# Kernel tuning notes

Measured on AMD Instinct MI355X. Metric: run time of the kernel, lower is better.

Reference implementation:

```python
import jax, jax.numpy as jnp
import numpy as np

EPS = 1e-6
ENERGY_THRESHOLD = 0.95
LS_INIT = 1e-5


def setup_inputs() -> dict:
    key = jax.random.key(0)
    k_x, k_u, k_s, k_v = jax.random.split(key, 4)
    dim, max_rank = 4096, 16
    x = jax.random.normal(k_x, (4, 2048, dim), dtype=jnp.float32)
    U = jax.random.normal(k_u, (dim, max_rank), dtype=jnp.float32) * 0.02
    S = jax.random.uniform(k_s, (max_rank,), dtype=jnp.float32)
    V = jax.random.normal(k_v, (max_rank, dim), dtype=jnp.float32) * 0.02
    norm_weight = jnp.ones((dim,), dtype=jnp.float32)
    gamma = jnp.full((dim,), LS_INIT, dtype=jnp.float32)
    return {"x": x, "U": U, "S": S, "V": V,
            "norm_weight": norm_weight, "gamma": gamma}


def _rank_mask(S):
    # Effective rank from singular-value energy (non-differentiable decision,
    # matching torch's .item() host sync which detaches it from autograd).
    s_abs = jnp.abs(S)
    cum = jnp.cumsum(s_abs) / jnp.maximum(s_abs.sum(), 1e-8)
    hit = cum >= ENERGY_THRESHOLD
    r = jnp.where(hit.any(), jnp.argmax(hit) + 1, S.shape[0])
    keep = (jnp.arange(S.shape[0]) < r).astype(S.dtype)
    return jax.lax.stop_gradient(keep)


def reference(x, U, S, V, norm_weight, gamma):
    # RMSNorm (computed in fp32, matching x.float() in torch)
    xf = x.astype(jnp.float32)
    x_norm = (xf * jax.lax.rsqrt(jnp.mean(xf * xf, axis=-1, keepdims=True) + EPS)).astype(x.dtype)
    x_norm = x_norm * norm_weight
    # Adaptive-rank low-rank projection: masking columns >= r equals slicing [:r]
    keep = _rank_mask(S)
    h = jnp.einsum('bsd,dr->bsr', x_norm, U)        # [B,S,max_rank]
    h = h * (S * keep)                               # zero out ranks >= r
    h = jnp.einsum('bsr,rd->bsd', h, V)             # [B,S,dim]
    # LayerScale + residual
    return x + h * gamma
```

## Files before the change

kernel.cpp:

```cpp
#include <hip/hip_runtime.h>

#define DIM   4096
#define RANK  16
#define ROWS  4
#define NT    512
#define NWAVE 8

typedef __fp16 f16;
typedef __fp16 f16x2 __attribute__((ext_vector_type(2)));
typedef __fp16 f16x4 __attribute__((ext_vector_type(4)));
typedef __fp16 f16x8 __attribute__((ext_vector_type(8)));
typedef int    int2v  __attribute__((ext_vector_type(2)));
typedef float  f32x4v __attribute__((ext_vector_type(4)));

__device__ __forceinline__ float fdot2f(f16x2 a, f16x2 b, float c) {
    return __builtin_amdgcn_fdot2(a, b, c, false);
}

__device__ __forceinline__ f16x2 h2get(const int4& v, int i) {
    int w;
    switch (i) { case 0: w = v.x; break; case 1: w = v.y; break;
                 case 2: w = v.z; break; default: w = v.w; }
    return __builtin_bit_cast(f16x2, w);
}

__global__ __launch_bounds__(256) void prep_weights(const float* __restrict__ U,
                                                    const float* __restrict__ nw,
                                                    const float* __restrict__ V,
                                                    f16* __restrict__ Ut,
                                                    f16* __restrict__ Vp) {
    const int d = blockIdx.x * 256 + threadIdx.x;
    const float wv = nw[d];
    const float4* U4 = (const float4*)U;
    const float4 u0 = U4[(size_t)d * 4 + 0];
    const float4 u1 = U4[(size_t)d * 4 + 1];
    const float4 u2 = U4[(size_t)d * 4 + 2];
    const float4 u3 = U4[(size_t)d * 4 + 3];
    Ut[ 0*DIM + d] = (f16)(u0.x*wv); Ut[ 1*DIM + d] = (f16)(u0.y*wv);
    Ut[ 2*DIM + d] = (f16)(u0.z*wv); Ut[ 3*DIM + d] = (f16)(u0.w*wv);
    Ut[ 4*DIM + d] = (f16)(u1.x*wv); Ut[ 5*DIM + d] = (f16)(u1.y*wv);
    Ut[ 6*DIM + d] = (f16)(u1.z*wv); Ut[ 7*DIM + d] = (f16)(u1.w*wv);
    Ut[ 8*DIM + d] = (f16)(u2.x*wv); Ut[ 9*DIM + d] = (f16)(u2.y*wv);
    Ut[10*DIM + d] = (f16)(u2.z*wv); Ut[11*DIM + d] = (f16)(u2.w*wv);
    Ut[12*DIM + d] = (f16)(u3.x*wv); Ut[13*DIM + d] = (f16)(u3.y*wv);
    Ut[14*DIM + d] = (f16)(u3.z*wv); Ut[15*DIM + d] = (f16)(u3.w*wv);
    f16 vq[16];
    #pragma unroll
    for (int q = 0; q < 16; ++q) vq[q] = (f16)V[(size_t)q * DIM + d];
    f16x8 lo = { vq[0], vq[1], vq[2], vq[3], vq[4], vq[5], vq[6], vq[7] };
    f16x8 hi = { vq[8], vq[9], vq[10], vq[11], vq[12], vq[13], vq[14], vq[15] };
    f16x8* Vp8 = (f16x8*)Vp;
    Vp8[(size_t)d * 2 + 0] = lo;
    Vp8[(size_t)d * 2 + 1] = hi;
}

__global__ __launch_bounds__(NT, 6) void arl_fused(
    const float* __restrict__ x,  const f16* __restrict__ Ut,
    const float* __restrict__ S,  const f16* __restrict__ Vp,
    const float* __restrict__ gamma, float* __restrict__ out)
{
    const int t    = threadIdx.x;
    const int w    = t >> 6;
    const int lane = t & 63;
    const int rg   = w & 3;
    const int dh   = w >> 2;
    const size_t row0 = (size_t)blockIdx.x * ROWS;

    const float4* x4   = (const float4*)(x + row0 * DIM);
    float4*       out4 = (float4*)(out + row0 * DIM);
    const int4*   Ut16 = (const int4*)Ut;
    const int4*   Vp16 = (const int4*)Vp;
    const float4* g4   = (const float4*)gamma;

    __shared__ __align__(16) f16 xh[ROWS * DIM];
    __shared__ float s_ssq[NWAVE][ROWS];
    __shared__ float s_hraw[NWAVE][16];
    __shared__ __align__(16) f16 s_hh[ROWS * RANK];

    float ssqp[ROWS] = {0.f, 0.f, 0.f, 0.f};
    #pragma unroll
    for (int i = 0; i < 8; ++i) {
        const int idx = i * NT + t;
        const int r   = i >> 1;
        const float4 val = x4[idx];
        ssqp[r] = fmaf(val.x, val.x, ssqp[r]);
        ssqp[r] = fmaf(val.y, val.y, ssqp[r]);
        ssqp[r] = fmaf(val.z, val.z, ssqp[r]);
        ssqp[r] = fmaf(val.w, val.w, ssqp[r]);
        f16x4 pk;
        pk.x = (f16)val.x; pk.y = (f16)val.y; pk.z = (f16)val.z; pk.w = (f16)val.w;
        ((f16x4*)xh)[idx] = pk;
    }
    __syncthreads();

    #pragma unroll
    for (int r = 0; r < ROWS; ++r) {
        float s = ssqp[r];
        #pragma unroll
        for (int off = 32; off >= 1; off >>= 1) s += __shfl_xor(s, off, 64);
        if (lane == 0) s_ssq[w][r] = s;
    }

    float v[16];
    #pragma unroll
    for (int i = 0; i < 16; ++i) v[i] = 0.f;

    #pragma unroll 1
    for (int k = 0; k < 4; ++k) {
        const int p = dh * 256 + k * 64 + lane;
        int4 u[4];
        #pragma unroll
        for (int ql = 0; ql < 4; ++ql)
            u[ql] = Ut16[(size_t)(rg * 4 + ql) * 512 + p];
        int4 xr[ROWS];
        #pragma unroll
        for (int r = 0; r < ROWS; ++r) xr[r] = ((const int4*)xh)[r * 512 + p];
        #pragma unroll
        for (int i = 0; i < 4; ++i) {
            f16x2 xp[ROWS];
            #pragma unroll
            for (int r = 0; r < ROWS; ++r) xp[r] = h2get(xr[r], i);
            #pragma unroll
            for (int ql = 0; ql < 4; ++ql) {
                const f16x2 up = h2get(u[ql], i);
                #pragma unroll
                for (int r = 0; r < ROWS; ++r)
                    v[r*4+ql] = fdot2f(xp[r], up, v[r*4+ql]);
            }
        }
    }

    #pragma unroll
    for (int i = 0; i < 8; ++i) {
        int a = __float_as_int(v[2*i]);
        int b = __float_as_int(v[2*i+1]);
        int2v pr = __builtin_amdgcn_permlane32_swap(a, b, false, false);
        v[i] = __int_as_float(pr.x) + __int_as_float(pr.y);
    }
    #pragma unroll
    for (int s = 1; s <= 3; ++s) {
        const int off = 32 >> s;
        const int n   = 8 >> s;
        const bool hi = (lane >> (5 - s)) & 1;
        #pragma unroll
        for (int i = 0; i < n; ++i) {
            float lo = v[2*i], hg = v[2*i+1];
            float slo = __shfl_xor(lo, off, 64);
            float shg = __shfl_xor(hg, off, 64);
            v[i] = hi ? (hg + shg) : (lo + slo);
        }
    }
    v[0] += __shfl_xor(v[0], 2, 64);
    v[0] += __shfl_xor(v[0], 1, 64);
    {
        const int idx = ((lane >> 5) & 1) | (((lane >> 4) & 1) << 1)
                      | (((lane >> 3) & 1) << 2) | (((lane >> 2) & 1) << 3);
        if ((lane & 3) == 0) s_hraw[w][idx] = v[0];
    }
    __syncthreads();

    if (t < 64) {
        const int r = t >> 4, q = t & 15;
        const int qg = q >> 2, ql = q & 3;
        const float hs = s_hraw[qg][r * 4 + ql] + s_hraw[qg + 4][r * 4 + ql];
        float tot_ssq = 0.f;
        #pragma unroll
        for (int ww = 0; ww < NWAVE; ++ww) tot_ssq += s_ssq[ww][r];
        const float rstd = rsqrtf(tot_ssq * (1.0f / DIM) + 1e-6f);
        float tot = 0.f;
        #pragma unroll
        for (int i = 0; i < RANK; ++i) tot += fabsf(S[i]);
        const float denom = fmaxf(tot, 1e-8f);
        float cum = 0.f, se = 0.f;
        #pragma unroll
        for (int i = 0; i < RANK; ++i) {
            if (i == q) se = ((cum / denom) < 0.95f) ? S[i] : 0.f;
            cum += fabsf(S[i]);
        }
        s_hh[t] = (f16)(hs * se * rstd);
    }
    __syncthreads();

    f16x2 hp[ROWS][8];
    {
        const int4* hh16 = (const int4*)s_hh;
        #pragma unroll
        for (int r = 0; r < ROWS; ++r) {
            const int4 a = hh16[r*2 + 0];
            const int4 b = hh16[r*2 + 1];
            #pragma unroll
            for (int i = 0; i < 4; ++i) {
                hp[r][i]     = h2get(a, i);
                hp[r][4 + i] = h2get(b, i);
            }
        }
    }
    #pragma unroll 1
    for (int k = 0; k < 2; ++k) {
        const int c = k * NT + t;
        float4 xr[ROWS];
        #pragma unroll
        for (int r = 0; r < ROWS; ++r) xr[r] = x4[(size_t)r * (DIM/4) + c];
        const float4 g = g4[c];
        float acc[ROWS][4];
        #pragma unroll
        for (int r = 0; r < ROWS; ++r)
            #pragma unroll
            for (int j = 0; j < 4; ++j) acc[r][j] = 0.f;
        #pragma unroll
        for (int j = 0; j < 4; ++j) {
            const int dd = c * 4 + j;
            const int4 v0 = Vp16[(size_t)dd * 2 + 0];
            const int4 v1 = Vp16[(size_t)dd * 2 + 1];
            #pragma unroll
            for (int r = 0; r < ROWS; ++r) {
                float a = acc[r][j];
                #pragma unroll
                for (int i = 0; i < 4; ++i)
                    a = fdot2f(hp[r][i], h2get(v0, i), a);
                #pragma unroll
                for (int i = 0; i < 4; ++i)
                    a = fdot2f(hp[r][4+i], h2get(v1, i), a);
                acc[r][j] = a;
            }
        }
        #pragma unroll
        for (int r = 0; r < ROWS; ++r) {
            float4 o;
            o.x = fmaf(g.x, acc[r][0], xr[r].x);
            o.y = fmaf(g.y, acc[r][1], xr[r].y);
            o.z = fmaf(g.z, acc[r][2], xr[r].z);
            o.w = fmaf(g.w, acc[r][3], xr[r].w);
            __builtin_nontemporal_store(*(const f32x4v*)&o,
                                        (f32x4v*)(out4 + (size_t)r * (DIM/4) + c));
        }
    }
}

extern "C" void kernel_launch(void* const* d_in, const int* in_sizes, int n_in,
                              void* d_out, int out_size, void* d_ws, size_t ws_size,
                              hipStream_t stream) {
    (void)in_sizes; (void)n_in; (void)ws_size;
    const float* x  = (const float*)d_in[0];
    const float* U  = (const float*)d_in[1];
    const float* S  = (const float*)d_in[2];
    const float* V  = (const float*)d_in[3];
    const float* nw = (const float*)d_in[4];
    const float* g  = (const float*)d_in[5];
    float* out = (float*)d_out;
    f16* Ut = (f16*)d_ws;
    f16* Vp = (f16*)((char*)d_ws + 16 * DIM * sizeof(f16));

    hipLaunchKernelGGL(prep_weights, dim3(DIM / 256), dim3(256), 0, stream,
                       U, nw, V, Ut, Vp);

    const int rows = out_size / DIM;
    const int grid = rows / ROWS;
    hipLaunchKernelGGL(arl_fused, dim3(grid), dim3(NT), 0, stream,
                       x, Ut, S, Vp, g, out);
}
```

Before: 85.33 us.

## Split fused kernel into projection and apply kernels, prefetch U tiles

Splits the single fused kernel in two. The first computes the normalized rank-16 projection h per row and writes it to a workspace. The second, with 256 threads per block, re-reads x and applies V, gamma and the residual. It also software-prefetches the next U tile inside the projection loop. The split is meant to free LDS and registers so more blocks fit per CU, at the cost of reading x from global memory a second time and adding a kernel launch.

New measurement: 87.41 us. 1.02x slower.

```diff
diff --git a/kernel.cpp b/kernel.cpp
--- a/kernel.cpp
+++ b/kernel.cpp
@@ -4,6 +4,7 @@
 #define RANK  16
 #define ROWS  4
 #define NT    512
+#define NTB   256
 #define NWAVE 8
 
 typedef __fp16 f16;
@@ -54,10 +55,9 @@
     Vp8[(size_t)d * 2 + 1] = hi;
 }
 
-__global__ __launch_bounds__(NT, 6) void arl_fused(
+__global__ __launch_bounds__(NT, 6) void arl_h(
     const float* __restrict__ x,  const f16* __restrict__ Ut,
-    const float* __restrict__ S,  const f16* __restrict__ Vp,
-    const float* __restrict__ gamma, float* __restrict__ out)
+    const float* __restrict__ S,  f16* __restrict__ hWS)
 {
     const int t    = threadIdx.x;
     const int w    = t >> 6;
@@ -67,15 +67,19 @@
     const size_t row0 = (size_t)blockIdx.x * ROWS;
 
     const float4* x4   = (const float4*)(x + row0 * DIM);
-    float4*       out4 = (float4*)(out + row0 * DIM);
     const int4*   Ut16 = (const int4*)Ut;
-    const int4*   Vp16 = (const int4*)Vp;
-    const float4* g4   = (const float4*)gamma;
 
     __shared__ __align__(16) f16 xh[ROWS * DIM];
     __shared__ float s_ssq[NWAVE][ROWS];
     __shared__ float s_hraw[NWAVE][16];
-    __shared__ __align__(16) f16 s_hh[ROWS * RANK];
+
+    int4 u[4];
+    {
+        const int p0 = dh * 256 + lane;
+        #pragma unroll
+        for (int ql = 0; ql < 4; ++ql)
+            u[ql] = Ut16[(size_t)(rg * 4 + ql) * 512 + p0];
+    }
 
     float ssqp[ROWS] = {0.f, 0.f, 0.f, 0.f};
     #pragma unroll
@@ -107,11 +111,12 @@
 
     #pragma unroll 1
     for (int k = 0; k < 4; ++k) {
+        const int pn = dh * 256 + ((k + 1) & 3) * 64 + lane;
+        int4 un[4];
+        #pragma unroll
+        for (int ql = 0; ql < 4; ++ql)
+            un[ql] = Ut16[(size_t)(rg * 4 + ql) * 512 + pn];
         const int p = dh * 256 + k * 64 + lane;
-        int4 u[4];
-        #pragma unroll
-        for (int ql = 0; ql < 4; ++ql)
-            u[ql] = Ut16[(size_t)(rg * 4 + ql) * 512 + p];
         int4 xr[ROWS];
         #pragma unroll
         for (int r = 0; r < ROWS; ++r) xr[r] = ((const int4*)xh)[r * 512 + p];
@@ -128,6 +133,8 @@
                     v[r*4+ql] = fdot2f(xp[r], up, v[r*4+ql]);
             }
         }
+        #pragma unroll
+        for (int ql = 0; ql < 4; ++ql) u[ql] = un[ql];
     }
 
     #pragma unroll
@@ -177,27 +184,39 @@
             if (i == q) se = ((cum / denom) < 0.95f) ? S[i] : 0.f;
             cum += fabsf(S[i]);
         }
-        s_hh[t] = (f16)(hs * se * rstd);
-    }
-    __syncthreads();
+        hWS[(row0 + r) * RANK + q] = (f16)(hs * se * rstd);
+    }
+}
+
+__global__ __launch_bounds__(NTB, 6) void arl_apply(
+    const float* __restrict__ x,  const f16* __restrict__ hWS,
+    const f16* __restrict__ Vp,   const float* __restrict__ gamma,
+    float* __restrict__ out)
+{
+    const int t = threadIdx.x;
+    const size_t row0 = (size_t)blockIdx.x * ROWS;
+
+    const float4* x4   = (const float4*)(x + row0 * DIM);
+    float4*       out4 = (float4*)(out + row0 * DIM);
+    const int4*   Vp16 = (const int4*)Vp;
+    const float4* g4   = (const float4*)gamma;
 
     f16x2 hp[ROWS][8];
-    {
-        const int4* hh16 = (const int4*)s_hh;
-        #pragma unroll
-        for (int r = 0; r < ROWS; ++r) {
-            const int4 a = hh16[r*2 + 0];
-            const int4 b = hh16[r*2 + 1];
-            #pragma unroll
-            for (int i = 0; i < 4; ++i) {
-                hp[r][i]     = h2get(a, i);
-                hp[r][4 + i] = h2get(b, i);
-            }
-        }
-    }
+    #pragma unroll
+    for (int r = 0; r < ROWS; ++r) {
+        const int4* hr = (const int4*)(hWS + (row0 + r) * RANK);
+        const int4 a = hr[0];
+        const int4 b = hr[1];
+        #pragma unroll
+        for (int i = 0; i < 4; ++i) {
+            hp[r][i]     = h2get(a, i);
+            hp[r][4 + i] = h2get(b, i);
+        }
+    }
+
     #pragma unroll 1
-    for (int k = 0; k < 2; ++k) {
-        const int c = k * NT + t;
+    for (int j = 0; j < 4; ++j) {
+        const int c = j * NTB + t;
         float4 xr[ROWS];
         #pragma unroll
         for (int r = 0; r < ROWS; ++r) xr[r] = x4[(size_t)r * (DIM/4) + c];
@@ -206,22 +225,22 @@
         #pragma unroll
         for (int r = 0; r < ROWS; ++r)
             #pragma unroll
-            for (int j = 0; j < 4; ++j) acc[r][j] = 0.f;
-        #pragma unroll
-        for (int j = 0; j < 4; ++j) {
-            const int dd = c * 4 + j;
+            for (int jj = 0; jj < 4; ++jj) acc[r][jj] = 0.f;
+        #pragma unroll
+        for (int jj = 0; jj < 4; ++jj) {
+            const int dd = c * 4 + jj;
             const int4 v0 = Vp16[(size_t)dd * 2 + 0];
             const int4 v1 = Vp16[(size_t)dd * 2 + 1];
             #pragma unroll
             for (int r = 0; r < ROWS; ++r) {
-                float a = acc[r][j];
+                float a = acc[r][jj];
                 #pragma unroll
                 for (int i = 0; i < 4; ++i)
                     a = fdot2f(hp[r][i], h2get(v0, i), a);
                 #pragma unroll
                 for (int i = 0; i < 4; ++i)
                     a = fdot2f(hp[r][4+i], h2get(v1, i), a);
-                acc[r][j] = a;
+                acc[r][jj] = a;
             }
         }
         #pragma unroll
@@ -248,14 +267,17 @@
     const float* nw = (const float*)d_in[4];
     const float* g  = (const float*)d_in[5];
     float* out = (float*)d_out;
-    f16* Ut = (f16*)d_ws;
-    f16* Vp = (f16*)((char*)d_ws + 16 * DIM * sizeof(f16));
+    f16* Ut  = (f16*)d_ws;
+    f16* Vp  = (f16*)((char*)d_ws + 128 * 1024);
+    f16* hWS = (f16*)((char*)d_ws + 256 * 1024);
 
     hipLaunchKernelGGL(prep_weights, dim3(DIM / 256), dim3(256), 0, stream,
                        U, nw, V, Ut, Vp);
 
     const int rows = out_size / DIM;
     const int grid = rows / ROWS;
-    hipLaunchKernelGGL(arl_fused, dim3(grid), dim3(NT), 0, stream,
-                       x, Ut, S, Vp, g, out);
-}
+    hipLaunchKernelGGL(arl_h, dim3(grid), dim3(NT), 0, stream,
+                       x, Ut, S, hWS);
+    hipLaunchKernelGGL(arl_apply, dim3(grid), dim3(NTB), 0, stream,
+                       x, hWS, Vp, g, out);
+}
```
